# Performance work log

Hardware: AMD Instinct MI355X
Metric: run time of the kernel (lower is better)

Reference implementation:

```python
import jax, jax.numpy as jnp
import numpy as np

NUM_HEADS = 8
NUM_GROUPS = 32
EPS = 1e-5

def group_norm(x, w, b):
    # x: [B, C, L]
    B, C, L = x.shape
    xg = x.reshape(B, NUM_GROUPS, C // NUM_GROUPS, L)
    mean = xg.mean(axis=(2, 3), keepdims=True)
    var = xg.var(axis=(2, 3), keepdims=True)
    xg = (xg - mean) * jax.lax.rsqrt(var + EPS)
    return xg.reshape(B, C, L) * w[None, :, None] + b[None, :, None]

def setup_inputs() -> dict:
    key = jax.random.key(0)
    ks = jax.random.split(key, 5)
    B, C, H, W = 16, 512, 32, 32
    x = jax.random.normal(ks[0], (B, C, H, W), dtype=jnp.float32)
    norm_w = jnp.ones((C,), dtype=jnp.float32)
    norm_b = jnp.zeros((C,), dtype=jnp.float32)
    w_qkv = jax.random.normal(ks[1], (3 * C, C), dtype=jnp.float32) * (1.0 / np.sqrt(C))
    b_qkv = jax.random.normal(ks[2], (3 * C,), dtype=jnp.float32) * 0.02
    w_proj = jax.random.normal(ks[3], (C, C), dtype=jnp.float32) * (1.0 / np.sqrt(C))
    b_proj = jax.random.normal(ks[4], (C,), dtype=jnp.float32) * 0.02
    return {"x": x, "norm_w": norm_w, "norm_b": norm_b, "w_qkv": w_qkv,
            "b_qkv": b_qkv, "w_proj": w_proj, "b_proj": b_proj}

def reference(x, norm_w, norm_b, w_qkv, b_qkv, w_proj, b_proj):
    B, C = x.shape[0], x.shape[1]
    L = int(np.prod(x.shape[2:]))
    xf = x.reshape(B, C, L)
    h = group_norm(xf, norm_w, norm_b)
    # 1x1 conv == channel matmul: [3C, C] x [B, C, L] -> [B, 3C, L]
    qkv = jnp.einsum('oc,bcl->bol', w_qkv, h) + b_qkv[None, :, None]
    ch = C // NUM_HEADS
    qkv = qkv.reshape(B * NUM_HEADS, 3 * ch, L)
    q, k, v = qkv[:, :ch], qkv[:, ch:2 * ch], qkv[:, 2 * ch:]
    scale = 1.0 / np.sqrt(np.sqrt(ch))
    weight = jnp.einsum('bct,bcs->bts', q * scale, k * scale)  # [B*H, L, L]
    weight = jax.nn.softmax(weight.astype(jnp.float32), axis=-1).astype(weight.dtype)
    a = jnp.einsum('bts,bcs->bct', weight, v)  # [B*H, ch, L]
    a = a.reshape(B, C, L)
    out = jnp.einsum('oc,bcl->bol', w_proj, a) + b_proj[None, :, None]
    return out  # [B, C, L]
```

## Files before the change

### kernel.cpp

```cpp
#include <hip/hip_runtime.h>
#include <math.h>


typedef _Float16 f16x8 __attribute__((ext_vector_type(8)));
typedef _Float16 f16x4 __attribute__((ext_vector_type(4)));
typedef float f32x4 __attribute__((ext_vector_type(4)));

#define MFMA_K16(A, B, C) __builtin_amdgcn_mfma_f32_16x16x16f16(A, B, C, 0, 0, 0)

__device__ __forceinline__ void async_cp16(const void* g, void* l) {
  __builtin_amdgcn_global_load_lds(
      (const __attribute__((address_space(1))) void*)g,
      (__attribute__((address_space(3))) void*)l, 16, 0, 0);
}

__global__ __launch_bounds__(256) void f32_to_f16(
    const float* __restrict__ src, _Float16* __restrict__ dst, int n4) {
  int i = blockIdx.x * 256 + threadIdx.x;
  if (i < n4) {
    float4 v = ((const float4*)src)[i];
    f16x4 o = {(_Float16)v.x, (_Float16)v.y, (_Float16)v.z, (_Float16)v.w};
    *(f16x4*)&dst[(size_t)i * 4] = o;
  }
}

__global__ __launch_bounds__(256) void gn_kernel(
    const float* __restrict__ x, const float* __restrict__ gw,
    const float* __restrict__ gb, _Float16* __restrict__ hT) {
  const int b = blockIdx.x >> 5;
  const int g = blockIdx.x & 31;
  const size_t base = ((size_t)(b * 512 + g * 16)) * 1024;
  const float4* xp = (const float4*)(x + base);
  const int tid = threadIdx.x;

  float4 vals[16];
  float s = 0.f, sq = 0.f;
#pragma unroll
  for (int r = 0; r < 16; ++r) {
    float4 v = xp[tid + 256 * r];
    vals[r] = v;
    s += v.x + v.y + v.z + v.w;
    sq += v.x * v.x + v.y * v.y + v.z * v.z + v.w * v.w;
  }
  __shared__ float rs[256];
  __shared__ float rq[256];
  rs[tid] = s;
  rq[tid] = sq;
  __syncthreads();
  for (int off = 128; off > 0; off >>= 1) {
    if (tid < off) {
      rs[tid] += rs[tid + off];
      rq[tid] += rq[tid + off];
    }
    __syncthreads();
  }
  const float mean = rs[0] * (1.f / 16384.f);
  const float var = rq[0] * (1.f / 16384.f) - mean * mean;
  const float rinv = rsqrtf(var + 1e-5f);
#pragma unroll
  for (int r = 0; r < 16; ++r) {
    const int c = g * 16 + r;
    const float wc = gw[c] * rinv;
    const float bc = gb[c] - mean * wc;
    vals[r].x = vals[r].x * wc + bc;
    vals[r].y = vals[r].y * wc + bc;
    vals[r].z = vals[r].z * wc + bc;
    vals[r].w = vals[r].w * wc + bc;
  }
  _Float16* hb = hT + ((size_t)b * 1024 + tid * 4) * 512 + g * 16;
#pragma unroll
  for (int li = 0; li < 4; ++li) {
    f16x8 o0, o1;
#pragma unroll
    for (int r = 0; r < 8; ++r) {
      float v0 = li == 0 ? vals[r].x : li == 1 ? vals[r].y
                 : li == 2 ? vals[r].z : vals[r].w;
      float v1 = li == 0 ? vals[8 + r].x : li == 1 ? vals[8 + r].y
                 : li == 2 ? vals[8 + r].z : vals[8 + r].w;
      o0[r] = (_Float16)v0;
      o1[r] = (_Float16)v1;
    }
    *(f16x8*)(hb + (size_t)li * 512) = o0;
    *(f16x8*)(hb + (size_t)li * 512 + 8) = o1;
  }
}

template <typename OutT, bool BIAS_ON_M>
__global__ __launch_bounds__(256) void gemm_tn(
    const _Float16* __restrict__ A, const _Float16* __restrict__ B,
    const float* __restrict__ bias, OutT* __restrict__ Out,
    int M, int N, int K, long sA, long sB) {
  __shared__ __align__(16) _Float16 As[128 * 32];
  __shared__ __align__(16) _Float16 Bs[128 * 32];
  const int tid = threadIdx.x;
  const int w = tid >> 6, lane = tid & 63;
  const int lx = lane & 15, quad = lane >> 4;
  const int wm = w >> 1, wn = w & 1;
  const int bn = blockIdx.x * 128, bm = blockIdx.y * 128;
  const int z = blockIdx.z;

  const int cr = w * 16;
  const int lrow = lane >> 2;
  const int lk = (lane & 3) * 8;
  const _Float16* Ag = A + (size_t)z * sA + (size_t)(bm + cr + lrow) * K + lk;
  const _Float16* Bg = B + (size_t)z * sB + (size_t)(bn + cr + lrow) * K + lk;
  _Float16* As0 = &As[cr * 32];
  _Float16* As1 = &As[(cr + 64) * 32];
  _Float16* Bs0 = &Bs[cr * 32];
  _Float16* Bs1 = &Bs[(cr + 64) * 32];

  f32x4 acc[4][4];
#pragma unroll
  for (int i = 0; i < 4; ++i)
#pragma unroll
    for (int j = 0; j < 4; ++j) acc[i][j] = (f32x4){0.f, 0.f, 0.f, 0.f};

  for (int k0 = 0; k0 < K; k0 += 32) {
    __syncthreads();
    async_cp16(Ag + k0, As0);
    async_cp16(Ag + (size_t)64 * K + k0, As1);
    async_cp16(Bg + k0, Bs0);
    async_cp16(Bg + (size_t)64 * K + k0, Bs1);
    __syncthreads();
    f16x8 af[4], bf[4];
#pragma unroll
    for (int mt = 0; mt < 4; ++mt)
      af[mt] = *(const f16x8*)&As[(wm * 64 + mt * 16 + lx) * 32 + quad * 8];
#pragma unroll
    for (int nt = 0; nt < 4; ++nt)
      bf[nt] = *(const f16x8*)&Bs[(wn * 64 + nt * 16 + lx) * 32 + quad * 8];
#pragma unroll
    for (int mt = 0; mt < 4; ++mt)
#pragma unroll
      for (int nt = 0; nt < 4; ++nt)
        acc[mt][nt] = __builtin_amdgcn_mfma_f32_16x16x32_f16(
            af[mt], bf[nt], acc[mt][nt], 0, 0, 0);
  }

  OutT* Ob = Out + (size_t)z * M * N;
#pragma unroll
  for (int mt = 0; mt < 4; ++mt) {
    const int m0 = bm + wm * 64 + mt * 16 + quad * 4;
    float bm4[4];
#pragma unroll
    for (int i = 0; i < 4; ++i) bm4[i] = BIAS_ON_M ? bias[m0 + i] : 0.f;
#pragma unroll
    for (int nt = 0; nt < 4; ++nt) {
      const int n = bn + wn * 64 + nt * 16 + lx;
      const float bn1 = BIAS_ON_M ? 0.f : bias[n];
      float v[4];
#pragma unroll
      for (int i = 0; i < 4; ++i)
        v[i] = acc[mt][nt][i] + (BIAS_ON_M ? bm4[i] : bn1);
      if constexpr (sizeof(OutT) == 2) {
        f16x4 o = {(_Float16)v[0], (_Float16)v[1], (_Float16)v[2],
                   (_Float16)v[3]};
        *(f16x4*)((_Float16*)Ob + (size_t)n * M + m0) = o;
      } else {
        float4 o = {v[0], v[1], v[2], v[3]};
        *(float4*)((float*)Ob + (size_t)n * M + m0) = o;
      }
    }
  }
}

#define LQ 72
#define LV 68

__global__ __launch_bounds__(256) void attn_mfma(
    const _Float16* __restrict__ qkvT, _Float16* __restrict__ aT) {
  __shared__ __align__(16) _Float16 ks[64 * LQ];
  __shared__ __align__(16) _Float16 vs[64 * LV];

  const int tid = threadIdx.x;
  const int w = tid >> 6, lane = tid & 63;
  const int lx = lane & 15, quad = lane >> 4;
  const int bh = blockIdx.y, b = bh >> 3, h = bh & 7;
  const int t0 = blockIdx.x * 64;
  const _Float16* qb = qkvT + (size_t)b * 1024 * 1536 + h * 192;

  const _Float16* qrow = qb + (size_t)(t0 + w * 16 + lx) * 1536;
  f16x8 qf0 = *(const f16x8*)(qrow + quad * 8);
  f16x8 qf1 = *(const f16x8*)(qrow + 32 + quad * 8);
#pragma unroll
  for (int j = 0; j < 8; ++j) {
    qf0[j] = qf0[j] * (_Float16)0.125f;
    qf1[j] = qf1[j] * (_Float16)0.125f;
  }

  float m_r = -1e30f, l_r = 0.f;
  f32x4 oacc[4];
#pragma unroll
  for (int mt = 0; mt < 4; ++mt) oacc[mt] = (f32x4){0.f, 0.f, 0.f, 0.f};

  for (int s0 = 0; s0 < 1024; s0 += 64) {
    __syncthreads();
    {
      const int r = tid >> 2, c = (tid & 3) * 16;
      const _Float16* g = qb + (size_t)(s0 + r) * 1536 + 64 + c;
      *(f16x8*)&ks[r * LQ + c] = *(const f16x8*)g;
      *(f16x8*)&ks[r * LQ + c + 8] = *(const f16x8*)(g + 8);
    }
    {
      const int s2 = (tid >> 3) * 2, c8 = (tid & 7) * 8;
      const _Float16* g = qb + (size_t)(s0 + s2) * 1536 + 128 + c8;
      f16x8 v0 = *(const f16x8*)g;
      f16x8 v1 = *(const f16x8*)(g + 1536);
#pragma unroll
      for (int i = 0; i < 8; ++i) {
        union { _Float16 hh[2]; unsigned u; } p;
        p.hh[0] = v0[i];
        p.hh[1] = v1[i];
        *(unsigned*)&vs[(c8 + i) * LV + s2] = p.u;
      }
    }
    __syncthreads();

    f32x4 sf[4];
#pragma unroll
    for (int sb = 0; sb < 4; ++sb) {
      f16x8 k0 = *(const f16x8*)&ks[(sb * 16 + lx) * LQ + quad * 8];
      f16x8 k1 = *(const f16x8*)&ks[(sb * 16 + lx) * LQ + 32 + quad * 8];
      f32x4 z = {0.f, 0.f, 0.f, 0.f};
      z = __builtin_amdgcn_mfma_f32_16x16x32_f16(k0, qf0, z, 0, 0, 0);
      sf[sb] = __builtin_amdgcn_mfma_f32_16x16x32_f16(k1, qf1, z, 0, 0, 0);
    }

    float mx = sf[0][0];
#pragma unroll
    for (int sb = 0; sb < 4; ++sb)
#pragma unroll
      for (int i = 0; i < 4; ++i) mx = fmaxf(mx, sf[sb][i]);
    mx = fmaxf(mx, __shfl_xor(mx, 16));
    mx = fmaxf(mx, __shfl_xor(mx, 32));
    const float mn = fmaxf(m_r, mx);
    const float alpha = __expf(m_r - mn);
    m_r = mn;
    float sum = 0.f;
    f16x4 pf[4];
#pragma unroll
    for (int sb = 0; sb < 4; ++sb) {
      float p0 = __expf(sf[sb][0] - mn);
      float p1 = __expf(sf[sb][1] - mn);
      float p2 = __expf(sf[sb][2] - mn);
      float p3 = __expf(sf[sb][3] - mn);
      sum += (p0 + p1) + (p2 + p3);
      pf[sb] = (f16x4){(_Float16)p0, (_Float16)p1, (_Float16)p2, (_Float16)p3};
    }
    sum += __shfl_xor(sum, 16);
    sum += __shfl_xor(sum, 32);
    l_r = l_r * alpha + sum;
    if (!__all(alpha == 1.f)) {
#pragma unroll
      for (int mt = 0; mt < 4; ++mt)
#pragma unroll
        for (int i = 0; i < 4; ++i) oacc[mt][i] *= alpha;
    }

#pragma unroll
    for (int kb = 0; kb < 4; ++kb)
#pragma unroll
      for (int mt = 0; mt < 4; ++mt) {
        f16x4 vf = *(const f16x4*)&vs[(mt * 16 + lx) * LV + kb * 16 + quad * 4];
        oacc[mt] = MFMA_K16(vf, pf[kb], oacc[mt]);
      }
  }

  const float linv = 1.f / l_r;
  _Float16* ob = aT + ((size_t)b * 1024 + t0 + w * 16 + lx) * 512 + h * 64;
#pragma unroll
  for (int mt = 0; mt < 4; ++mt) {
    f16x4 o = {(_Float16)(oacc[mt][0] * linv), (_Float16)(oacc[mt][1] * linv),
               (_Float16)(oacc[mt][2] * linv), (_Float16)(oacc[mt][3] * linv)};
    *(f16x4*)&ob[mt * 16 + quad * 4] = o;
  }
}

extern "C" void kernel_launch(void* const* d_in, const int* in_sizes, int n_in,
                              void* d_out, int out_size, void* d_ws,
                              size_t ws_size, hipStream_t stream) {
  const float* x = (const float*)d_in[0];
  const float* norm_w = (const float*)d_in[1];
  const float* norm_b = (const float*)d_in[2];
  const float* w_qkv = (const float*)d_in[3];
  const float* b_qkv = (const float*)d_in[4];
  const float* w_proj = (const float*)d_in[5];
  const float* b_proj = (const float*)d_in[6];
  float* out = (float*)d_out;

  _Float16* hT = (_Float16*)d_ws;
  _Float16* qkvT = hT + (size_t)16 * 1024 * 512;
  _Float16* wq = qkvT + (size_t)16 * 1024 * 1536;
  _Float16* wp = wq + (size_t)1536 * 512;
  _Float16* aT = hT;

  f32_to_f16<<<768, 256, 0, stream>>>(w_qkv, wq, 196608);
  f32_to_f16<<<256, 256, 0, stream>>>(w_proj, wp, 65536);
  gn_kernel<<<512, 256, 0, stream>>>(x, norm_w, norm_b, hT);
  gemm_tn<_Float16, true><<<dim3(8, 12, 16), 256, 0, stream>>>(
      wq, hT, b_qkv, qkvT, 1536, 1024, 512, 0L, 524288L);
  attn_mfma<<<dim3(16, 128), 256, 0, stream>>>(qkvT, aT);
  gemm_tn<float, false><<<dim3(4, 8, 16), 256, 0, stream>>>(
      aT, wp, b_proj, out, 1024, 512, 512, 524288L, 0L);
}
```

Baseline: 244.5 us.

## Stage GEMM epilogue through LDS and process two query tiles per attention warp

The GEMM epilogue now writes the accumulator tile into shared memory and then issues fully coalesced 16-byte row stores, where before it wrote scattered 4-element column chunks. The attention kernel now handles 128 queries per block, two 16-row groups per warp, so each K/V tile loaded into LDS serves twice as many queries and global K/V traffic is halved. The trade-offs are more registers, fewer attention blocks (1024), and extra LDS round-trips and barriers in the epilogue.

```diff
diff --git a/kernel.cpp b/kernel.cpp
--- a/kernel.cpp
+++ b/kernel.cpp
@@ -90,8 +90,9 @@
     const _Float16* __restrict__ A, const _Float16* __restrict__ B,
     const float* __restrict__ bias, OutT* __restrict__ Out,
     int M, int N, int K, long sA, long sB) {
-  __shared__ __align__(16) _Float16 As[128 * 32];
-  __shared__ __align__(16) _Float16 Bs[128 * 32];
+  __shared__ __align__(16) char smem[34816];
+  _Float16* As = (_Float16*)smem;
+  _Float16* Bs = As + 128 * 32;
   const int tid = threadIdx.x;
   const int w = tid >> 6, lane = tid & 63;
   const int lx = lane & 15, quad = lane >> 4;
@@ -138,27 +139,64 @@
   }
 
   OutT* Ob = Out + (size_t)z * M * N;
-#pragma unroll
-  for (int mt = 0; mt < 4; ++mt) {
-    const int m0 = bm + wm * 64 + mt * 16 + quad * 4;
-    float bm4[4];
-#pragma unroll
-    for (int i = 0; i < 4; ++i) bm4[i] = BIAS_ON_M ? bias[m0 + i] : 0.f;
-#pragma unroll
-    for (int nt = 0; nt < 4; ++nt) {
-      const int n = bn + wn * 64 + nt * 16 + lx;
-      const float bn1 = BIAS_ON_M ? 0.f : bias[n];
-      float v[4];
-#pragma unroll
-      for (int i = 0; i < 4; ++i)
-        v[i] = acc[mt][nt][i] + (BIAS_ON_M ? bm4[i] : bn1);
-      if constexpr (sizeof(OutT) == 2) {
-        f16x4 o = {(_Float16)v[0], (_Float16)v[1], (_Float16)v[2],
-                   (_Float16)v[3]};
-        *(f16x4*)((_Float16*)Ob + (size_t)n * M + m0) = o;
-      } else {
-        float4 o = {v[0], v[1], v[2], v[3]};
-        *(float4*)((float*)Ob + (size_t)n * M + m0) = o;
+  if constexpr (sizeof(OutT) == 2) {
+    _Float16* T = (_Float16*)smem;
+    __syncthreads();
+#pragma unroll
+    for (int mt = 0; mt < 4; ++mt) {
+      const int m0 = bm + wm * 64 + mt * 16 + quad * 4;
+      float bm4[4];
+#pragma unroll
+      for (int i = 0; i < 4; ++i) bm4[i] = BIAS_ON_M ? bias[m0 + i] : 0.f;
+#pragma unroll
+      for (int nt = 0; nt < 4; ++nt) {
+        const int nl = wn * 64 + nt * 16 + lx;
+        const float bn1 = BIAS_ON_M ? 0.f : bias[bn + nl];
+        f16x4 o = {(_Float16)(acc[mt][nt][0] + (BIAS_ON_M ? bm4[0] : bn1)),
+                   (_Float16)(acc[mt][nt][1] + (BIAS_ON_M ? bm4[1] : bn1)),
+                   (_Float16)(acc[mt][nt][2] + (BIAS_ON_M ? bm4[2] : bn1)),
+                   (_Float16)(acc[mt][nt][3] + (BIAS_ON_M ? bm4[3] : bn1))};
+        *(f16x4*)&T[nl * 136 + wm * 64 + mt * 16 + quad * 4] = o;
+      }
+    }
+    __syncthreads();
+#pragma unroll
+    for (int j = 0; j < 8; ++j) {
+      const int r = j * 16 + (tid >> 4), slot = tid & 15;
+      f16x8 vv = *(const f16x8*)&T[r * 136 + slot * 8];
+      *(f16x8*)((_Float16*)Ob + (size_t)(bn + r) * M + bm + slot * 8) = vv;
+    }
+  } else {
+    float* T32 = (float*)smem;
+#pragma unroll
+    for (int p = 0; p < 2; ++p) {
+      __syncthreads();
+      if (wn == p) {
+#pragma unroll
+        for (int mt = 0; mt < 4; ++mt) {
+          const int m0 = bm + wm * 64 + mt * 16 + quad * 4;
+          float bm4[4];
+#pragma unroll
+          for (int i = 0; i < 4; ++i) bm4[i] = BIAS_ON_M ? bias[m0 + i] : 0.f;
+#pragma unroll
+          for (int nt = 0; nt < 4; ++nt) {
+            const int nl = nt * 16 + lx;
+            const float bn1 = BIAS_ON_M ? 0.f : bias[bn + p * 64 + nl];
+            float4 o = {acc[mt][nt][0] + (BIAS_ON_M ? bm4[0] : bn1),
+                        acc[mt][nt][1] + (BIAS_ON_M ? bm4[1] : bn1),
+                        acc[mt][nt][2] + (BIAS_ON_M ? bm4[2] : bn1),
+                        acc[mt][nt][3] + (BIAS_ON_M ? bm4[3] : bn1)};
+            *(float4*)&T32[nl * 136 + wm * 64 + mt * 16 + quad * 4] = o;
+          }
+        }
+      }
+      __syncthreads();
+#pragma unroll
+      for (int j = 0; j < 8; ++j) {
+        const int r = j * 8 + (tid >> 5), slot = tid & 31;
+        float4 vv = *(const float4*)&T32[r * 136 + slot * 4];
+        *(float4*)((float*)Ob + (size_t)(bn + p * 64 + r) * M + bm + slot * 4) =
+            vv;
       }
     }
   }
@@ -176,22 +214,28 @@
   const int w = tid >> 6, lane = tid & 63;
   const int lx = lane & 15, quad = lane >> 4;
   const int bh = blockIdx.y, b = bh >> 3, h = bh & 7;
-  const int t0 = blockIdx.x * 64;
+  const int t0 = blockIdx.x * 128;
   const _Float16* qb = qkvT + (size_t)b * 1024 * 1536 + h * 192;
 
-  const _Float16* qrow = qb + (size_t)(t0 + w * 16 + lx) * 1536;
-  f16x8 qf0 = *(const f16x8*)(qrow + quad * 8);
-  f16x8 qf1 = *(const f16x8*)(qrow + 32 + quad * 8);
-#pragma unroll
-  for (int j = 0; j < 8; ++j) {
-    qf0[j] = qf0[j] * (_Float16)0.125f;
-    qf1[j] = qf1[j] * (_Float16)0.125f;
-  }
-
-  float m_r = -1e30f, l_r = 0.f;
-  f32x4 oacc[4];
-#pragma unroll
-  for (int mt = 0; mt < 4; ++mt) oacc[mt] = (f32x4){0.f, 0.f, 0.f, 0.f};
+  f16x8 qf[2][2];
+#pragma unroll
+  for (int g = 0; g < 2; ++g) {
+    const _Float16* qrow = qb + (size_t)(t0 + w * 32 + g * 16 + lx) * 1536;
+    qf[g][0] = *(const f16x8*)(qrow + quad * 8);
+    qf[g][1] = *(const f16x8*)(qrow + 32 + quad * 8);
+#pragma unroll
+    for (int j = 0; j < 8; ++j) {
+      qf[g][0][j] = qf[g][0][j] * (_Float16)0.125f;
+      qf[g][1][j] = qf[g][1][j] * (_Float16)0.125f;
+    }
+  }
+
+  float m_r[2] = {-1e30f, -1e30f}, l_r[2] = {0.f, 0.f};
+  f32x4 oacc[2][4];
+#pragma unroll
+  for (int g = 0; g < 2; ++g)
+#pragma unroll
+    for (int mt = 0; mt < 4; ++mt) oacc[g][mt] = (f32x4){0.f, 0.f, 0.f, 0.f};
 
   for (int s0 = 0; s0 < 1024; s0 += 64) {
     __syncthreads();
@@ -216,45 +260,53 @@
     }
     __syncthreads();
 
-    f32x4 sf[4];
+    f32x4 sf[2][4];
 #pragma unroll
     for (int sb = 0; sb < 4; ++sb) {
       f16x8 k0 = *(const f16x8*)&ks[(sb * 16 + lx) * LQ + quad * 8];
       f16x8 k1 = *(const f16x8*)&ks[(sb * 16 + lx) * LQ + 32 + quad * 8];
-      f32x4 z = {0.f, 0.f, 0.f, 0.f};
-      z = __builtin_amdgcn_mfma_f32_16x16x32_f16(k0, qf0, z, 0, 0, 0);
-      sf[sb] = __builtin_amdgcn_mfma_f32_16x16x32_f16(k1, qf1, z, 0, 0, 0);
-    }
-
-    float mx = sf[0][0];
-#pragma unroll
-    for (int sb = 0; sb < 4; ++sb)
-#pragma unroll
-      for (int i = 0; i < 4; ++i) mx = fmaxf(mx, sf[sb][i]);
-    mx = fmaxf(mx, __shfl_xor(mx, 16));
-    mx = fmaxf(mx, __shfl_xor(mx, 32));
-    const float mn = fmaxf(m_r, mx);
-    const float alpha = __expf(m_r - mn);
-    m_r = mn;
-    float sum = 0.f;
-    f16x4 pf[4];
-#pragma unroll
-    for (int sb = 0; sb < 4; ++sb) {
-      float p0 = __expf(sf[sb][0] - mn);
-      float p1 = __expf(sf[sb][1] - mn);
-      float p2 = __expf(sf[sb][2] - mn);
-      float p3 = __expf(sf[sb][3] - mn);
-      sum += (p0 + p1) + (p2 + p3);
-      pf[sb] = (f16x4){(_Float16)p0, (_Float16)p1, (_Float16)p2, (_Float16)p3};
-    }
-    sum += __shfl_xor(sum, 16);
-    sum += __shfl_xor(sum, 32);
-    l_r = l_r * alpha + sum;
-    if (!__all(alpha == 1.f)) {
-#pragma unroll
-      for (int mt = 0; mt < 4; ++mt)
-#pragma unroll
-        for (int i = 0; i < 4; ++i) oacc[mt][i] *= alpha;
+#pragma unroll
+      for (int g = 0; g < 2; ++g) {
+        f32x4 z = {0.f, 0.f, 0.f, 0.f};
+        z = __builtin_amdgcn_mfma_f32_16x16x32_f16(k0, qf[g][0], z, 0, 0, 0);
+        sf[g][sb] =
+            __builtin_amdgcn_mfma_f32_16x16x32_f16(k1, qf[g][1], z, 0, 0, 0);
+      }
+    }
+
+    f16x4 pf[2][4];
+#pragma unroll
+    for (int g = 0; g < 2; ++g) {
+      float mx = sf[g][0][0];
+#pragma unroll
+      for (int sb = 0; sb < 4; ++sb)
+#pragma unroll
+        for (int i = 0; i < 4; ++i) mx = fmaxf(mx, sf[g][sb][i]);
+      mx = fmaxf(mx, __shfl_xor(mx, 16));
+      mx = fmaxf(mx, __shfl_xor(mx, 32));
+      const float mn = fmaxf(m_r[g], mx);
+      const float alpha = __expf(m_r[g] - mn);
+      m_r[g] = mn;
+      float sum = 0.f;
+#pragma unroll
+      for (int sb = 0; sb < 4; ++sb) {
+        float p0 = __expf(sf[g][sb][0] - mn);
+        float p1 = __expf(sf[g][sb][1] - mn);
+        float p2 = __expf(sf[g][sb][2] - mn);
+        float p3 = __expf(sf[g][sb][3] - mn);
+        sum += (p0 + p1) + (p2 + p3);
+        pf[g][sb] =
+            (f16x4){(_Float16)p0, (_Float16)p1, (_Float16)p2, (_Float16)p3};
+      }
+      sum += __shfl_xor(sum, 16);
+      sum += __shfl_xor(sum, 32);
+      l_r[g] = l_r[g] * alpha + sum;
+      if (!__all(alpha == 1.f)) {
+#pragma unroll
+        for (int mt = 0; mt < 4; ++mt)
+#pragma unroll
+          for (int i = 0; i < 4; ++i) oacc[g][mt][i] *= alpha;
+      }
     }
 
 #pragma unroll
@@ -262,17 +314,24 @@
 #pragma unroll
       for (int mt = 0; mt < 4; ++mt) {
         f16x4 vf = *(const f16x4*)&vs[(mt * 16 + lx) * LV + kb * 16 + quad * 4];
-        oacc[mt] = MFMA_K16(vf, pf[kb], oacc[mt]);
-      }
-  }
-
-  const float linv = 1.f / l_r;
-  _Float16* ob = aT + ((size_t)b * 1024 + t0 + w * 16 + lx) * 512 + h * 64;
-#pragma unroll
-  for (int mt = 0; mt < 4; ++mt) {
-    f16x4 o = {(_Float16)(oacc[mt][0] * linv), (_Float16)(oacc[mt][1] * linv),
-               (_Float16)(oacc[mt][2] * linv), (_Float16)(oacc[mt][3] * linv)};
-    *(f16x4*)&ob[mt * 16 + quad * 4] = o;
+        oacc[0][mt] = MFMA_K16(vf, pf[0][kb], oacc[0][mt]);
+        oacc[1][mt] = MFMA_K16(vf, pf[1][kb], oacc[1][mt]);
+      }
+  }
+
+#pragma unroll
+  for (int g = 0; g < 2; ++g) {
+    const float linv = 1.f / l_r[g];
+    _Float16* ob =
+        aT + ((size_t)b * 1024 + t0 + w * 32 + g * 16 + lx) * 512 + h * 64;
+#pragma unroll
+    for (int mt = 0; mt < 4; ++mt) {
+      f16x4 o = {(_Float16)(oacc[g][mt][0] * linv),
+                 (_Float16)(oacc[g][mt][1] * linv),
+                 (_Float16)(oacc[g][mt][2] * linv),
+                 (_Float16)(oacc[g][mt][3] * linv)};
+      *(f16x4*)&ob[mt * 16 + quad * 4] = o;
+    }
   }
 }
 
@@ -299,7 +358,7 @@
   gn_kernel<<<512, 256, 0, stream>>>(x, norm_w, norm_b, hT);
   gemm_tn<_Float16, true><<<dim3(8, 12, 16), 256, 0, stream>>>(
       wq, hT, b_qkv, qkvT, 1536, 1024, 512, 0L, 524288L);
-  attn_mfma<<<dim3(16, 128), 256, 0, stream>>>(qkvT, aT);
+  attn_mfma<<<dim3(8, 128), 256, 0, stream>>>(qkvT, aT);
   gemm_tn<float, false><<<dim3(4, 8, 16), 256, 0, stream>>>(
       aT, wp, b_proj, out, 1024, 512, 512, 524288L, 0L);
 }
```

After: 242.3 us. Within noise of the previous version (-0.9%).
